# Kernel optimization log

Measured on AMD Instinct MI355X. Metric: run time of the kernel, lower is better.

## Reference

```python
import jax, jax.numpy as jnp
import numpy as np

QMAX = 127.0  # int8 symmetric range


def _fake_quant(x, axes):
    """AQT-style int8 symmetric fake-quant over contraction axes.

    Returns quantized integer values (stored as f32) and per-channel scales
    (keepdims over `axes`).
    """
    absmax = jnp.max(jnp.abs(x), axis=axes, keepdims=True)
    scale = jnp.where(absmax > 0, absmax / QMAX, jnp.ones_like(absmax))
    q = jnp.clip(jnp.round(x / scale), -QMAX, QMAX)
    return q, scale


def setup_inputs() -> dict:
    key = jax.random.key(0)
    k1, k2 = jax.random.split(key)
    lhs = jax.random.normal(k1, (4, 16384, 512), dtype=jnp.float32)
    rhs = jax.random.normal(k2, (512, 512), dtype=jnp.float32)
    return {"lhs": lhs, "rhs": rhs}


def reference(lhs, rhs):
    # dimension_numbers = (((2,), (0,)), ((), ())) -- Dense-style contraction.
    # Quantize each operand symmetrically to int8 along its contraction axis.
    lhs_q, lhs_scale = _fake_quant(lhs, axes=(2,))   # lhs_q: [B,S,D], scale: [B,S,1]
    rhs_q, rhs_scale = _fake_quant(rhs, axes=(0,))   # rhs_q: [D,F], scale: [1,F]
    # Integer-valued matmul (accumulation exact in f32 for these magnitudes),
    # then dequantize with the outer product of scales.
    acc = jnp.einsum('bsd,df->bsf', lhs_q, rhs_q)    # [B,S,F]
    return acc * lhs_scale * rhs_scale               # broadcast [B,S,1]*[1,F]
```

## Files before the change

kernel.cpp:

```cpp
#include <hip/hip_runtime.h>
#include <hip/hip_bf16.h>
#include <stdint.h>

#define QMAX 127.0f

typedef __attribute__((ext_vector_type(4))) int   i32x4;
typedef __attribute__((ext_vector_type(2))) int   i32x2;
typedef __attribute__((ext_vector_type(4))) float f32x4v;

typedef __attribute__((address_space(1))) const void GVoid;
typedef __attribute__((address_space(3))) void LVoid;

__device__ inline int quant_i(float x, float inv) {
    float q = rintf(x * inv);
    q = fminf(fmaxf(q, -QMAX), QMAX);
    return (int)q;
}

__device__ inline uint32_t pack4(f32x4v v, float inv) {
    return (uint32_t)(quant_i(v.x, inv) & 255)
         | ((uint32_t)(quant_i(v.y, inv) & 255) << 8)
         | ((uint32_t)(quant_i(v.z, inv) & 255) << 16)
         | ((uint32_t)(quant_i(v.w, inv) & 255) << 24);
}

__device__ inline float amax8(f32x4v a, f32x4v b) {
    return fmaxf(fmaxf(fmaxf(fabsf(a.x), fabsf(a.y)), fmaxf(fabsf(a.z), fabsf(a.w))),
                 fmaxf(fmaxf(fabsf(b.x), fabsf(b.y)), fmaxf(fabsf(b.z), fabsf(b.w))));
}

__global__ __launch_bounds__(256, 8) void quant_kernel(const float* __restrict__ lhs,
                                                       const float* __restrict__ rhs,
                                                       int8_t* __restrict__ Aq,
                                                       int8_t* __restrict__ Btf,
                                                       float* __restrict__ lscale,
                                                       float* __restrict__ rscale,
                                                       int nLhs) {
    const int lane = threadIdx.x & 63;
    const int wave = threadIdx.x >> 6;
    const int bid  = blockIdx.x;

    if (bid >= nLhs) {
        const int f = (bid - nLhs) * 4 + wave;
        float v[8];
        float amax = 0.f;
#pragma unroll
        for (int i = 0; i < 8; ++i) {
            v[i] = rhs[(size_t)(lane + 64 * i) * 512 + f];
            amax = fmaxf(amax, fabsf(v[i]));
        }
#pragma unroll
        for (int m = 1; m <= 32; m <<= 1)
            amax = fmaxf(amax, __shfl_xor(amax, m, 64));
        const float inv = amax > 0.f ? QMAX / amax : 0.f;
        if (lane == 0) rscale[f] = amax > 0.f ? amax * (1.0f / QMAX) : 1.0f;
        const int laneHi = lane >> 4, lane15 = lane & 15;
        const int fbase = (f >> 4) * 1024 + (f & 15) * 16 + laneHi * 256 + lane15;
#pragma unroll
        for (int i = 0; i < 8; ++i)
            Btf[i * 32768 + fbase] = (int8_t)quant_i(v[i], inv);
        return;
    }

    const int row0 = bid * 32 + wave * 8;
    const float* rp = lhs + (size_t)row0 * 512 + lane * 8;
    int8_t* op = Aq + (size_t)row0 * 512 + lane * 8;
#pragma unroll
    for (int r = 0; r < 8; r += 2) {
        const f32x4v a0 = __builtin_nontemporal_load((const f32x4v*)(rp + (size_t)r * 512));
        const f32x4v b0 = __builtin_nontemporal_load((const f32x4v*)(rp + (size_t)r * 512 + 4));
        const f32x4v a1 = __builtin_nontemporal_load((const f32x4v*)(rp + (size_t)(r + 1) * 512));
        const f32x4v b1 = __builtin_nontemporal_load((const f32x4v*)(rp + (size_t)(r + 1) * 512 + 4));
        float m0 = amax8(a0, b0);
        float m1 = amax8(a1, b1);
#pragma unroll
        for (int m = 1; m <= 32; m <<= 1) {
            m0 = fmaxf(m0, __shfl_xor(m0, m, 64));
            m1 = fmaxf(m1, __shfl_xor(m1, m, 64));
        }
        const float inv0 = m0 > 0.f ? QMAX / m0 : 0.f;
        const float inv1 = m1 > 0.f ? QMAX / m1 : 0.f;
        if (lane == 0) {
            lscale[row0 + r]     = m0 > 0.f ? m0 * (1.0f / QMAX) : 1.0f;
            lscale[row0 + r + 1] = m1 > 0.f ? m1 * (1.0f / QMAX) : 1.0f;
        }
        i32x2 p0, p1;
        p0.x = (int)pack4(a0, inv0); p0.y = (int)pack4(b0, inv0);
        p1.x = (int)pack4(a1, inv1); p1.y = (int)pack4(b1, inv1);
        *(i32x2*)(op + (size_t)r * 512)       = p0;
        *(i32x2*)(op + (size_t)(r + 1) * 512) = p1;
    }
}

__global__ __launch_bounds__(256, 3) void gemm_kernel(const int8_t* __restrict__ Aq,
                                                      const int8_t* __restrict__ Btf,
                                                      const float* __restrict__ lscale,
                                                      const float* __restrict__ rscale,
                                                      float* __restrict__ out) {
    __shared__ int8_t lds[32768];

    const int tid  = threadIdx.x;
    const int lane = tid & 63;
    const int wave = tid >> 6;
    const int wr   = wave >> 1;
    const int wc   = wave & 1;

    const int g   = blockIdx.x;
    const int xcd = g & 7;
    const int j   = g >> 3;
    const int m0  = (xcd * 64 + (j >> 2)) * 128;
    const int n0  = (j & 3) * 128;

    i32x4 acc[4][4];
#pragma unroll
    for (int i = 0; i < 4; ++i)
#pragma unroll
        for (int jj = 0; jj < 4; ++jj)
            acc[i][jj] = (i32x4){0, 0, 0, 0};

    const int lane15 = lane & 15;
    const int laneHi = lane >> 4;
    const int8_t* bbase = Btf + (size_t)(n0 >> 4) * 1024 + (size_t)wc * 4096 + lane * 16;

#define STAGE_A(KT, BUF)                                                            \
    {                                                                               \
        _Pragma("unroll")                                                           \
        for (int c = 0; c < 4; ++c) {                                               \
            const int chunk = (c * 4 + wave) * 1024;                                \
            const int d     = chunk + lane * 16;                                    \
            const int row   = d >> 7;                                               \
            const int srck  = (d & 127) ^ ((row & 7) << 4);                         \
            const int8_t* sA = Aq + (size_t)(m0 + row) * 512 + (KT) + srck;         \
            __builtin_amdgcn_global_load_lds((GVoid*)sA, (LVoid*)(lds + (BUF) + chunk), 16, 0, 0); \
        }                                                                           \
    }

    STAGE_A(0, 0)

#pragma unroll
    for (int t = 0; t < 4; ++t) {
        const int buf = (t & 1) * 16384;
        if (t < 3) {
            STAGE_A((t + 1) * 128, ((t + 1) & 1) * 16384)
            asm volatile("s_waitcnt vmcnt(4)" ::: "memory");
        } else {
            asm volatile("s_waitcnt vmcnt(0)" ::: "memory");
        }
        __builtin_amdgcn_s_barrier();
        __builtin_amdgcn_sched_barrier(0);

        i32x4 af[4][2], bf[4][2];
#pragma unroll
        for (int ni = 0; ni < 4; ++ni)
#pragma unroll
            for (int kk = 0; kk < 2; ++kk)
                bf[ni][kk] = *(const i32x4*)(bbase + (size_t)(t * 2 + kk) * 32768 + ni * 1024);
#pragma unroll
        for (int mi = 0; mi < 4; ++mi) {
            const int row = wr * 64 + mi * 16 + lane15;
            const int sw  = (row & 7) << 4;
#pragma unroll
            for (int kk = 0; kk < 2; ++kk) {
                const int kb = kk * 64 + laneHi * 16;
                af[mi][kk] = *(const i32x4*)(lds + buf + row * 128 + (kb ^ sw));
            }
        }
#pragma unroll
        for (int kk = 0; kk < 2; ++kk)
#pragma unroll
            for (int mi = 0; mi < 4; ++mi)
#pragma unroll
                for (int ni = 0; ni < 4; ++ni)
                    acc[mi][ni] = __builtin_amdgcn_mfma_i32_16x16x64_i8(
                        af[mi][kk], bf[ni][kk], acc[mi][ni], 0, 0, 0);

        if (t < 3) __builtin_amdgcn_s_barrier();
    }
#undef STAGE_A

    float rs[4];
#pragma unroll
    for (int ni = 0; ni < 4; ++ni)
        rs[ni] = rscale[n0 + wc * 64 + ni * 16 + lane15];
    const int rg = laneHi * 4;
#pragma unroll
    for (int mi = 0; mi < 4; ++mi) {
#pragma unroll
        for (int r = 0; r < 4; ++r) {
            const int grow = m0 + wr * 64 + mi * 16 + rg + r;
            const float ls = lscale[grow];
            float* op = out + (size_t)grow * 512 + n0 + wc * 64;
#pragma unroll
            for (int ni = 0; ni < 4; ++ni)
                op[ni * 16 + lane15] = (float)acc[mi][ni][r] * ls * rs[ni];
        }
    }
}

extern "C" void kernel_launch(void* const* d_in, const int* in_sizes, int n_in,
                              void* d_out, int out_size, void* d_ws, size_t ws_size,
                              hipStream_t stream) {
    const float* lhs = (const float*)d_in[0];
    const float* rhs = (const float*)d_in[1];
    float* out = (float*)d_out;

    char* ws = (char*)d_ws;
    int8_t* Btf   = (int8_t*)ws;
    float* rscale = (float*)(ws + 262144);
    float* lscale = (float*)(ws + 266240);
    int8_t* Aq    = (int8_t*)(ws + 1048576);

    const int rows = in_sizes[0] / 512;
    const int nLhs = rows / 32;

    quant_kernel<<<nLhs + 128, 256, 0, stream>>>(lhs, rhs, Aq, Btf, lscale, rscale, nLhs);
    gemm_kernel<<<(rows / 128) * 4, 256, 0, stream>>>(Aq, Btf, lscale, rscale, out);
}
```

Measured before the change: 72.13 us.

## Retile GEMM to 64x256 blocks with full-K A tile loaded once

The GEMM block tile changes from 128x128 to 64x256. The whole 64x512 int8 A slab is loaded into LDS in one shot, followed by a single barrier, so the double-buffered per-K pipeline and its per-step barriers are removed. Each wave now owns a 64-column strip and reads B fragments straight from global memory across 8 K-steps. This cuts sync overhead and A traffic, but global loads no longer overlap with MFMA inside a block, and each block holds a 32KB LDS buffer.

```diff
diff --git a/kernel.cpp b/kernel.cpp
--- a/kernel.cpp
+++ b/kernel.cpp
@@ -97,19 +97,33 @@
                                                       const float* __restrict__ lscale,
                                                       const float* __restrict__ rscale,
                                                       float* __restrict__ out) {
-    __shared__ int8_t lds[32768];
+    __shared__ int8_t A[32768];
 
     const int tid  = threadIdx.x;
     const int lane = tid & 63;
     const int wave = tid >> 6;
-    const int wr   = wave >> 1;
-    const int wc   = wave & 1;
 
     const int g   = blockIdx.x;
     const int xcd = g & 7;
     const int j   = g >> 3;
-    const int m0  = (xcd * 64 + (j >> 2)) * 128;
-    const int n0  = (j & 3) * 128;
+    const int m0  = (xcd * 128 + (j >> 1)) * 64;
+    const int n0  = (j & 1) * 256;
+
+#pragma unroll
+    for (int c = 0; c < 8; ++c) {
+        const int chunk = (c * 4 + wave) * 1024;
+        const int d     = chunk + lane * 16;
+        const int row   = d >> 9;
+        const int srck  = (d & 511) ^ ((row & 7) << 4);
+        const int8_t* sA = Aq + (size_t)(m0 + row) * 512 + srck;
+        __builtin_amdgcn_global_load_lds((GVoid*)sA, (LVoid*)(A + chunk), 16, 0, 0);
+    }
+    __syncthreads();
+
+    const int lane15  = lane & 15;
+    const int laneHi  = lane >> 4;
+    const int colBase = n0 + wave * 64;
+    const int8_t* bbase = Btf + (size_t)(colBase >> 4) * 1024 + lane * 16;
 
     i32x4 acc[4][4];
 #pragma unroll
@@ -118,78 +132,38 @@
         for (int jj = 0; jj < 4; ++jj)
             acc[i][jj] = (i32x4){0, 0, 0, 0};
 
-    const int lane15 = lane & 15;
-    const int laneHi = lane >> 4;
-    const int8_t* bbase = Btf + (size_t)(n0 >> 4) * 1024 + (size_t)wc * 4096 + lane * 16;
-
-#define STAGE_A(KT, BUF)                                                            \
-    {                                                                               \
-        _Pragma("unroll")                                                           \
-        for (int c = 0; c < 4; ++c) {                                               \
-            const int chunk = (c * 4 + wave) * 1024;                                \
-            const int d     = chunk + lane * 16;                                    \
-            const int row   = d >> 7;                                               \
-            const int srck  = (d & 127) ^ ((row & 7) << 4);                         \
-            const int8_t* sA = Aq + (size_t)(m0 + row) * 512 + (KT) + srck;         \
-            __builtin_amdgcn_global_load_lds((GVoid*)sA, (LVoid*)(lds + (BUF) + chunk), 16, 0, 0); \
-        }                                                                           \
-    }
-
-    STAGE_A(0, 0)
-
 #pragma unroll
-    for (int t = 0; t < 4; ++t) {
-        const int buf = (t & 1) * 16384;
-        if (t < 3) {
-            STAGE_A((t + 1) * 128, ((t + 1) & 1) * 16384)
-            asm volatile("s_waitcnt vmcnt(4)" ::: "memory");
-        } else {
-            asm volatile("s_waitcnt vmcnt(0)" ::: "memory");
-        }
-        __builtin_amdgcn_s_barrier();
-        __builtin_amdgcn_sched_barrier(0);
-
-        i32x4 af[4][2], bf[4][2];
+    for (int ks = 0; ks < 8; ++ks) {
+        i32x4 bf[4], af[4];
 #pragma unroll
         for (int ni = 0; ni < 4; ++ni)
-#pragma unroll
-            for (int kk = 0; kk < 2; ++kk)
-                bf[ni][kk] = *(const i32x4*)(bbase + (size_t)(t * 2 + kk) * 32768 + ni * 1024);
+            bf[ni] = *(const i32x4*)(bbase + (size_t)ks * 32768 + ni * 1024);
 #pragma unroll
         for (int mi = 0; mi < 4; ++mi) {
-            const int row = wr * 64 + mi * 16 + lane15;
-            const int sw  = (row & 7) << 4;
-#pragma unroll
-            for (int kk = 0; kk < 2; ++kk) {
-                const int kb = kk * 64 + laneHi * 16;
-                af[mi][kk] = *(const i32x4*)(lds + buf + row * 128 + (kb ^ sw));
-            }
+            const int row = mi * 16 + lane15;
+            const int kb  = row * 512 + ks * 64 + laneHi * 16;
+            af[mi] = *(const i32x4*)(A + (kb ^ ((row & 7) << 4)));
         }
 #pragma unroll
-        for (int kk = 0; kk < 2; ++kk)
+        for (int mi = 0; mi < 4; ++mi)
 #pragma unroll
-            for (int mi = 0; mi < 4; ++mi)
-#pragma unroll
-                for (int ni = 0; ni < 4; ++ni)
-                    acc[mi][ni] = __builtin_amdgcn_mfma_i32_16x16x64_i8(
-                        af[mi][kk], bf[ni][kk], acc[mi][ni], 0, 0, 0);
-
-        if (t < 3) __builtin_amdgcn_s_barrier();
+            for (int ni = 0; ni < 4; ++ni)
+                acc[mi][ni] = __builtin_amdgcn_mfma_i32_16x16x64_i8(
+                    af[mi], bf[ni], acc[mi][ni], 0, 0, 0);
     }
-#undef STAGE_A
 
     float rs[4];
 #pragma unroll
     for (int ni = 0; ni < 4; ++ni)
-        rs[ni] = rscale[n0 + wc * 64 + ni * 16 + lane15];
+        rs[ni] = rscale[colBase + ni * 16 + lane15];
     const int rg = laneHi * 4;
 #pragma unroll
     for (int mi = 0; mi < 4; ++mi) {
 #pragma unroll
         for (int r = 0; r < 4; ++r) {
-            const int grow = m0 + wr * 64 + mi * 16 + rg + r;
+            const int grow = m0 + mi * 16 + rg + r;
             const float ls = lscale[grow];
-            float* op = out + (size_t)grow * 512 + n0 + wc * 64;
+            float* op = out + (size_t)grow * 512 + colBase;
 #pragma unroll
             for (int ni = 0; ni < 4; ++ni)
                 op[ni * 16 + lane15] = (float)acc[mi][ni][r] * ls * rs[ni];
@@ -214,5 +188,5 @@
     const int nLhs = rows / 32;
 
     quant_kernel<<<nLhs + 128, 256, 0, stream>>>(lhs, rhs, Aq, Btf, lscale, rscale, nLhs);
-    gemm_kernel<<<(rows / 128) * 4, 256, 0, stream>>>(Aq, Btf, lscale, rscale, out);
+    gemm_kernel<<<(rows / 64) * 2, 256, 0, stream>>>(Aq, Btf, lscale, rscale, out);
 }
```

After: 75.42 us. 1.05x slower.
